# Kernel optimization log

Measured on AMD Instinct MI355X. Metric: run time of the kernel, lower is better.

The kernel has to match this reference:

```python
import jax, jax.numpy as jnp
import numpy as np

NUM_FEATURE = 50


def setup_inputs() -> dict:
    key = jax.random.key(0)
    k1, k2 = jax.random.split(key)
    query = jax.random.normal(k1, (512, NUM_FEATURE), dtype=jnp.float32)
    doc = jax.random.normal(k2, (512, 256, NUM_FEATURE), dtype=jnp.float32)
    # nn.Linear(150, 1, bias=False) with weight filled with 1
    W = jnp.ones((3 * NUM_FEATURE,), dtype=jnp.float32)
    return {"query": query, "doc": doc, "W": W}


def reference(query, doc, W):
    # Split the single 150-dim linear weight into the three trilinear parts:
    # score(x, y) = w1.sen_x + w2.q_y + w3.(sen_x * q_y)
    w1, w2, w3 = W[:NUM_FEATURE], W[NUM_FEATURE:2 * NUM_FEATURE], W[2 * NUM_FEATURE:]
    q_term = query @ w2                      # [Lq]
    qw3 = query * w3                         # [Lq, d]

    def per_sentence(sen):                   # sen: [Ls, d]
        sXY = (sen @ w1)[:, None] + q_term[None, :] + sen @ qw3.T   # [Ls, Lq]
        sD2Q = jax.nn.softmax(sXY, axis=0)   # softmax over sentence tokens
        sQ2D = jax.nn.softmax(sXY, axis=1)   # softmax over query tokens
        aD2Q = sD2Q @ query                  # [Ls, d]
        aQ2D = sD2Q @ (sQ2D.T @ sen)         # (sD2Q @ sQ2D.T) @ sen, cheaper order
        return jnp.concatenate([sen, aD2Q, sen * aD2Q, sen * aQ2D], axis=1)  # [Ls, 4d]

    return jax.vmap(per_sentence)(doc)       # [n_sen, Ls, 4d]
```

## Files before the change

### kernel.cpp

```cpp
#include <hip/hip_runtime.h>
#include <math.h>

typedef __bf16 bf16_t;
typedef bf16_t bf16x2 __attribute__((ext_vector_type(2)));
typedef bf16_t bf16x4 __attribute__((ext_vector_type(4)));
typedef bf16_t bf16x8 __attribute__((ext_vector_type(8)));
typedef float f32x4 __attribute__((ext_vector_type(4)));

#define MFMA16(a,b,c) __builtin_amdgcn_mfma_f32_16x16x32_bf16((a),(b),(c),0,0,0)

#define ND 256
#define NQ 512
#define NF 50
#define L2E 1.44269504f
#define SHIFT 64.0f

#define SENT_E 0
#define PD0_E  16896
#define PD1_E  35328
#define QW3_E  53760
#define QTT_E  62976
#define KL0_E  16896
#define KL1_E  27136
#define EA_B   74752
#define PART_B  144384
#define STATS_B 148480
#define LDS_BYTES 151808

#define ST_QTERM 0
#define ST_CI    512
#define ST_RINV  576

__launch_bounds__(1024, 4)
__global__ void ca10_kernel(const float* __restrict__ query,
                            const float* __restrict__ doc,
                            const float* __restrict__ W,
                            float* __restrict__ out)
{
    extern __shared__ char smem[];
    bf16_t* lb = (bf16_t*)smem;
    float* part  = (float*)(smem + PART_B);
    float* stats = (float*)(smem + STATS_B);

    const int tid = threadIdx.x;
    const int w = tid >> 6, l = tid & 63, ln = l & 15, lg = l >> 4;
    const int s = blockIdx.x;
    const float* sen_g = doc + (size_t)s * (ND * NF);

    auto stageQW3 = [&](int jt, int buf, int tbase, int tn) {
        const int j0 = jt * 64;
        bf16_t* dst = lb + QW3_E + buf * 4608;
        for (int e = tid - tbase; e < 1664; e += tn) {
            int jj = e / 26, c = e - jj * 26;
            if (c < 25) {
                float2 v = ((const float2*)query)[(j0 + jj) * 25 + c];
                bf16x2 p;
                p[0] = (bf16_t)(v.x * W[100 + 2 * c] * L2E);
                p[1] = (bf16_t)(v.y * W[100 + 2 * c + 1] * L2E);
                *(bf16x2*)&dst[jj * 72 + 2 * c] = p;
            } else {
                bf16x2 p;
                p[0] = (bf16_t)(stats[ST_QTERM + j0 + jj] * L2E);
                p[1] = (bf16_t)L2E;
                *(bf16x2*)&dst[jj * 72 + 50] = p;
            }
        }
    };
    auto stageQTT = [&](int jt, int buf, int tbase, int tn) {
        const int j0 = jt * 64;
        bf16_t* dst = lb + QTT_E + buf * 4608;
        for (int e = tid - tbase; e < 1600; e += tn) {
            int c = e >> 6, jj = e & 63;
            float2 v = ((const float2*)query)[(j0 + jj) * 25 + c];
            dst[(2 * c) * 72 + jj]     = (bf16_t)v.x;
            dst[(2 * c + 1) * 72 + jj] = (bf16_t)v.y;
        }
    };

    for (int e = tid; e < 924; e += 1024) {
        int f = 50 + e / 66, c4 = (e - (e / 66) * 66) * 4;
        *(bf16x4*)&lb[SENT_E + f * 264 + c4] = (bf16x4){(bf16_t)0.f,(bf16_t)0.f,(bf16_t)0.f,(bf16_t)0.f};
    }
    for (int e = tid; e < 768; e += 1024) {
        int i = e / 3, c4 = 52 + (e - (e / 3) * 3) * 4;
        *(bf16x4*)&lb[PD0_E + i * 72 + c4] = (bf16x4){(bf16_t)0.f,(bf16_t)0.f,(bf16_t)0.f,(bf16_t)0.f};
    }
    for (int e = tid; e < 384; e += 1024) {
        int b = e / 192, r = e - b * 192;
        int jj = r / 3, c4 = 52 + (r - (r / 3) * 3) * 4;
        *(bf16x4*)&lb[QW3_E + b * 4608 + jj * 72 + c4] = (bf16x4){(bf16_t)0.f,(bf16_t)0.f,(bf16_t)0.f,(bf16_t)0.f};
    }
    for (int e = tid; e < 504; e += 1024) {
        int b = e / 252, r = e - b * 252;
        int f = 50 + r / 18, c4 = (r - (r / 18) * 18) * 4;
        *(bf16x4*)&lb[QTT_E + b * 4608 + f * 72 + c4] = (bf16x4){(bf16_t)0.f,(bf16_t)0.f,(bf16_t)0.f,(bf16_t)0.f};
    }
    for (int e = tid; e < 256 * 25; e += 1024) {
        int i = e / 25, c = e - i * 25;
        float2 v = ((const float2*)sen_g)[i * 25 + c];
        bf16x2 p; p[0] = (bf16_t)v.x; p[1] = (bf16_t)v.y;
        *(bf16x2*)&lb[PD0_E + i * 72 + 2 * c] = p;
        lb[SENT_E + (2 * c) * 264 + i]     = p[0];
        lb[SENT_E + (2 * c + 1) * 264 + i] = p[1];
    }
    if (tid < NQ) {
        float acc = 0.f;
        #pragma unroll
        for (int c = 0; c < 25; ++c) {
            float2 v = ((const float2*)query)[tid * 25 + c];
            acc += v.x * W[NF + 2 * c] + v.y * W[NF + 2 * c + 1];
        }
        stats[ST_QTERM + tid] = acc;
    }
    if (tid < ND) {
        float acc = 0.f;
        #pragma unroll
        for (int f = 0; f < NF; ++f) acc += sen_g[tid * NF + f] * W[f];
        lb[PD0_E + tid * 72 + 50] = (bf16_t)1.0f;
        lb[PD0_E + tid * 72 + 51] = (bf16_t)acc;
    }
    __syncthreads();

    bf16x8 aS[2];
    #pragma unroll
    for (int ks = 0; ks < 2; ++ks)
        aS[ks] = *(bf16x8*)&lb[PD0_E + (w * 16 + ln) * 72 + lg * 8 + ks * 32];
    stageQW3(0, 0, 0, 1024);
    stageQTT(0, 0, 0, 1024);
    __syncthreads();

    f32x4 accD[4];
    f32x4 K[9];
    #pragma unroll
    for (int nf = 0; nf < 4; ++nf) accD[nf] = (f32x4){0.f, 0.f, 0.f, 0.f};
    #pragma unroll
    for (int d = 0; d < 9; ++d) K[d] = (f32x4){0.f, 0.f, 0.f, 0.f};
    float rpart[4] = {0.f, 0.f, 0.f, 0.f};

    auto consumeTile = [&](const bf16_t* pdp, const bf16_t* qtp) {
        bf16x8 aPs[2];
        #pragma unroll
        for (int ks = 0; ks < 2; ++ks) {
            bf16x8 raw = *(bf16x8*)&pdp[(w * 16 + ln) * 72 + lg * 8 + ks * 32];
            float4 c0 = *(const float4*)&stats[ST_CI + lg * 8 + ks * 32];
            float4 c1 = *(const float4*)&stats[ST_CI + lg * 8 + ks * 32 + 4];
            aPs[ks][0] = (bf16_t)((float)raw[0] * c0.x);
            aPs[ks][1] = (bf16_t)((float)raw[1] * c0.y);
            aPs[ks][2] = (bf16_t)((float)raw[2] * c0.z);
            aPs[ks][3] = (bf16_t)((float)raw[3] * c0.w);
            aPs[ks][4] = (bf16_t)((float)raw[4] * c1.x);
            aPs[ks][5] = (bf16_t)((float)raw[5] * c1.y);
            aPs[ks][6] = (bf16_t)((float)raw[6] * c1.z);
            aPs[ks][7] = (bf16_t)((float)raw[7] * c1.w);
        }
        #pragma unroll
        for (int ks = 0; ks < 2; ++ks)
            #pragma unroll
            for (int nf = 0; nf < 4; ++nf) {
                bf16x8 bq = *(bf16x8*)&qtp[(nf * 16 + ln) * 72 + lg * 8 + ks * 32];
                accD[nf] = MFMA16(aPs[ks], bq, accD[nf]);
            }
        #pragma unroll
        for (int d = 0; d < 9; ++d) {
            if (d < 8 || w < 8) {
                const int cb = (w + d) & 15;
                #pragma unroll
                for (int ks = 0; ks < 2; ++ks) {
                    bf16x8 bb = *(bf16x8*)&pdp[(cb * 16 + ln) * 72 + lg * 8 + ks * 32];
                    K[d] = MFMA16(aPs[ks], bb, K[d]);
                }
            }
        }
    };

    for (int jt = 0; jt < 8; ++jt) {
        if (jt > 0) {
            const int pb = (jt - 1) & 1;
            consumeTile(lb + (pb ? PD1_E : PD0_E), lb + QTT_E + pb * 4608);
        }

        const bf16_t* qb = lb + QW3_E + (jt & 1) * 4608;
        bf16_t* pd = lb + ((jt & 1) ? PD1_E : PD0_E);
        #pragma unroll
        for (int hf = 0; hf < 2; ++hf) {
            f32x4 acc[2];
            acc[0] = (f32x4){-SHIFT, -SHIFT, -SHIFT, -SHIFT};
            acc[1] = (f32x4){-SHIFT, -SHIFT, -SHIFT, -SHIFT};
            #pragma unroll
            for (int ks = 0; ks < 2; ++ks)
                #pragma unroll
                for (int h = 0; h < 2; ++h) {
                    const int nf = hf * 2 + h;
                    bf16x8 b = *(bf16x8*)&qb[(nf * 16 + ln) * 72 + lg * 8 + ks * 32];
                    acc[h] = MFMA16(aS[ks], b, acc[h]);
                }
            #pragma unroll
            for (int h = 0; h < 2; ++h) {
                const int nf = hf * 2 + h;
                #pragma unroll
                for (int r = 0; r < 4; ++r) acc[h][r] = exp2f(acc[h][r]);
                float cp = (acc[h][0] + acc[h][1]) + (acc[h][2] + acc[h][3]);
                cp += __shfl_xor(cp, 16);
                cp += __shfl_xor(cp, 32);
                if (lg == 0) part[w * 64 + nf * 16 + ln] = cp;
                #pragma unroll
                for (int r = 0; r < 4; ++r) {
                    rpart[r] += acc[h][r];
                    pd[(w * 16 + lg * 4 + r) * 72 + nf * 16 + ln] = (bf16_t)acc[h][r];
                }
            }
        }
        __syncthreads();

        if (w == 0) {
            float cs = 0.f;
            #pragma unroll
            for (int ww = 0; ww < 16; ++ww) cs += part[ww * 64 + l];
            stats[ST_CI + l] = 1.f / cs;
        } else if (jt < 7) {
            stageQW3(jt + 1, (jt + 1) & 1, 64, 960);
            stageQTT(jt + 1, (jt + 1) & 1, 64, 960);
        }
        __syncthreads();
    }
    consumeTile(lb + PD1_E, lb + QTT_E + 4608);

    #pragma unroll
    for (int r = 0; r < 4; ++r) {
        float v = rpart[r];
        v += __shfl_xor(v, 1);
        v += __shfl_xor(v, 2);
        v += __shfl_xor(v, 4);
        v += __shfl_xor(v, 8);
        if (ln == 0) stats[ST_RINV + w * 16 + lg * 4 + r] = 1.f / v;
    }
    __syncthreads();

    float* ea = (float*)(smem + EA_B);
    #pragma unroll
    for (int nf = 0; nf < 4; ++nf)
        #pragma unroll
        for (int r = 0; r < 4; ++r)
            ea[(w * 16 + lg * 4 + r) * 68 + nf * 16 + ln] = accD[nf][r];

    f32x4 accQ[4];
    #pragma unroll
    for (int nf = 0; nf < 4; ++nf) accQ[nf] = (f32x4){0.f, 0.f, 0.f, 0.f};
    #pragma unroll
    for (int kt = 0; kt < 8; ++kt) {
        bf16_t* kl = lb + ((kt & 1) ? KL1_E : KL0_E);
        #pragma unroll
        for (int d = 0; d < 9; ++d) {
            if (d < 8 || w < 8) {
                const int cb = (w + d) & 15;
                if ((cb >> 1) == kt) {
                    const int h = cb & 1;
                    const float riv = stats[ST_RINV + cb * 16 + ln];
                    #pragma unroll
                    for (int r = 0; r < 4; ++r)
                        kl[(w * 16 + lg * 4 + r) * 40 + h * 16 + ln] =
                            (bf16_t)(K[d][r] * riv);
                }
            }
        }
        if ((w >> 1) == kt) {
            const int h = w & 1;
            float4 rv = *(const float4*)&stats[ST_RINV + w * 16 + lg * 4];
            #pragma unroll
            for (int d = 1; d < 9; ++d) {
                if (d < 8 || w < 8) {
                    const int cb = (w + d) & 15;
                    bf16x4 pk;
                    pk[0] = (bf16_t)(K[d][0] * rv.x);
                    pk[1] = (bf16_t)(K[d][1] * rv.y);
                    pk[2] = (bf16_t)(K[d][2] * rv.z);
                    pk[3] = (bf16_t)(K[d][3] * rv.w);
                    *(bf16x4*)&kl[(cb * 16 + ln) * 40 + h * 16 + lg * 4] = pk;
                }
            }
        }
        __syncthreads();
        bf16x8 aK = *(bf16x8*)&kl[(w * 16 + ln) * 40 + lg * 8];
        #pragma unroll
        for (int nf = 0; nf < 4; ++nf) {
            bf16x8 b = *(bf16x8*)&lb[SENT_E + (nf * 16 + ln) * 264 + kt * 32 + lg * 8];
            accQ[nf] = MFMA16(aK, b, accQ[nf]);
        }
    }
    __syncthreads();

    float* eb = (float*)smem;
    #pragma unroll
    for (int nf = 0; nf < 4; ++nf)
        #pragma unroll
        for (int r = 0; r < 4; ++r)
            eb[(w * 16 + lg * 4 + r) * 68 + nf * 16 + ln] = accQ[nf][r];
    __syncthreads();
    const size_t ob0 = (size_t)s * (ND * 200);
    #pragma unroll
    for (int seg = 0; seg < 4; ++seg) {
        for (int v = tid; v < 6400; v += 1024) {
            int i = v / 25, c = v - (v / 25) * 25;
            int f = 2 * c;
            float2 o;
            if (seg == 0) {
                o = *(const float2*)&sen_g[i * 50 + f];
            } else if (seg == 1) {
                o.x = ea[i * 68 + f]; o.y = ea[i * 68 + f + 1];
            } else if (seg == 2) {
                float2 d = *(const float2*)&sen_g[i * 50 + f];
                o.x = d.x * ea[i * 68 + f]; o.y = d.y * ea[i * 68 + f + 1];
            } else {
                float2 d = *(const float2*)&sen_g[i * 50 + f];
                o.x = d.x * eb[i * 68 + f]; o.y = d.y * eb[i * 68 + f + 1];
            }
            *(float2*)&out[ob0 + (size_t)i * 200 + seg * 50 + f] = o;
        }
    }
}

extern "C" void kernel_launch(void* const* d_in, const int* in_sizes, int n_in,
                              void* d_out, int out_size, void* d_ws, size_t ws_size,
                              hipStream_t stream) {
    const float* query = (const float*)d_in[0];
    const float* doc   = (const float*)d_in[1];
    const float* W     = (const float*)d_in[2];
    float* out = (float*)d_out;
    (void)d_ws; (void)ws_size; (void)n_in; (void)in_sizes; (void)out_size;

    hipFuncSetAttribute((const void*)ca10_kernel,
                        hipFuncAttributeMaxDynamicSharedMemorySize,
                        LDS_BYTES);
    ca10_kernel<<<dim3(512), dim3(1024), LDS_BYTES, stream>>>(query, doc, W, out);
}
```

Measured before the change: 139.1 us.

## Halve block to 8 waves, each computing two 16-row M fragments

Moves from 16 waves handling 16 rows each to 8 waves handling 32 rows each. Every B fragment loaded from LDS now feeds two MFMAs, roughly halving LDS reads per MFMA, and the symmetric K-matrix tiling is regrouped into 32x32 block pairs. The cost is higher register pressure per wave (more accumulators) and fewer waves to hide latency, since LDS use still limits the CU to one block.

```diff
diff --git a/kernel.cpp b/kernel.cpp
--- a/kernel.cpp
+++ b/kernel.cpp
@@ -31,8 +31,8 @@
 #define ST_CI    512
 #define ST_RINV  576
 
-__launch_bounds__(1024, 4)
-__global__ void ca10_kernel(const float* __restrict__ query,
+__launch_bounds__(512, 2)
+__global__ void ca11_kernel(const float* __restrict__ query,
                             const float* __restrict__ doc,
                             const float* __restrict__ W,
                             float* __restrict__ out)
@@ -77,25 +77,25 @@
         }
     };
 
-    for (int e = tid; e < 924; e += 1024) {
+    for (int e = tid; e < 924; e += 512) {
         int f = 50 + e / 66, c4 = (e - (e / 66) * 66) * 4;
         *(bf16x4*)&lb[SENT_E + f * 264 + c4] = (bf16x4){(bf16_t)0.f,(bf16_t)0.f,(bf16_t)0.f,(bf16_t)0.f};
     }
-    for (int e = tid; e < 768; e += 1024) {
+    for (int e = tid; e < 768; e += 512) {
         int i = e / 3, c4 = 52 + (e - (e / 3) * 3) * 4;
         *(bf16x4*)&lb[PD0_E + i * 72 + c4] = (bf16x4){(bf16_t)0.f,(bf16_t)0.f,(bf16_t)0.f,(bf16_t)0.f};
     }
-    for (int e = tid; e < 384; e += 1024) {
+    for (int e = tid; e < 384; e += 512) {
         int b = e / 192, r = e - b * 192;
         int jj = r / 3, c4 = 52 + (r - (r / 3) * 3) * 4;
         *(bf16x4*)&lb[QW3_E + b * 4608 + jj * 72 + c4] = (bf16x4){(bf16_t)0.f,(bf16_t)0.f,(bf16_t)0.f,(bf16_t)0.f};
     }
-    for (int e = tid; e < 504; e += 1024) {
+    for (int e = tid; e < 504; e += 512) {
         int b = e / 252, r = e - b * 252;
         int f = 50 + r / 18, c4 = (r - (r / 18) * 18) * 4;
         *(bf16x4*)&lb[QTT_E + b * 4608 + f * 72 + c4] = (bf16x4){(bf16_t)0.f,(bf16_t)0.f,(bf16_t)0.f,(bf16_t)0.f};
     }
-    for (int e = tid; e < 256 * 25; e += 1024) {
+    for (int e = tid; e < 256 * 25; e += 512) {
         int i = e / 25, c = e - i * 25;
         float2 v = ((const float2*)sen_g)[i * 25 + c];
         bf16x2 p; p[0] = (bf16_t)v.x; p[1] = (bf16_t)v.y;
@@ -103,7 +103,7 @@
         lb[SENT_E + (2 * c) * 264 + i]     = p[0];
         lb[SENT_E + (2 * c + 1) * 264 + i] = p[1];
     }
-    if (tid < NQ) {
+    {
         float acc = 0.f;
         #pragma unroll
         for (int c = 0; c < 25; ++c) {
@@ -121,53 +121,70 @@
     }
     __syncthreads();
 
-    bf16x8 aS[2];
-    #pragma unroll
-    for (int ks = 0; ks < 2; ++ks)
-        aS[ks] = *(bf16x8*)&lb[PD0_E + (w * 16 + ln) * 72 + lg * 8 + ks * 32];
-    stageQW3(0, 0, 0, 1024);
-    stageQTT(0, 0, 0, 1024);
-    __syncthreads();
-
-    f32x4 accD[4];
-    f32x4 K[9];
-    #pragma unroll
-    for (int nf = 0; nf < 4; ++nf) accD[nf] = (f32x4){0.f, 0.f, 0.f, 0.f};
-    #pragma unroll
-    for (int d = 0; d < 9; ++d) K[d] = (f32x4){0.f, 0.f, 0.f, 0.f};
-    float rpart[4] = {0.f, 0.f, 0.f, 0.f};
+    bf16x8 aS[2][2];
+    #pragma unroll
+    for (int mf = 0; mf < 2; ++mf)
+        #pragma unroll
+        for (int ks = 0; ks < 2; ++ks)
+            aS[mf][ks] = *(bf16x8*)&lb[PD0_E + (w * 32 + mf * 16 + ln) * 72 + lg * 8 + ks * 32];
+    stageQW3(0, 0, 0, 512);
+    stageQTT(0, 0, 0, 512);
+    __syncthreads();
+
+    f32x4 accD[2][4];
+    f32x4 K[5][2][2];
+    #pragma unroll
+    for (int mf = 0; mf < 2; ++mf)
+        #pragma unroll
+        for (int nf = 0; nf < 4; ++nf) accD[mf][nf] = (f32x4){0.f, 0.f, 0.f, 0.f};
+    #pragma unroll
+    for (int e = 0; e < 5; ++e)
+        #pragma unroll
+        for (int mf = 0; mf < 2; ++mf)
+            #pragma unroll
+            for (int b = 0; b < 2; ++b) K[e][mf][b] = (f32x4){0.f, 0.f, 0.f, 0.f};
+    float rpart[2][4] = {{0.f,0.f,0.f,0.f},{0.f,0.f,0.f,0.f}};
 
     auto consumeTile = [&](const bf16_t* pdp, const bf16_t* qtp) {
-        bf16x8 aPs[2];
+        bf16x8 aPs[2][2];
         #pragma unroll
         for (int ks = 0; ks < 2; ++ks) {
-            bf16x8 raw = *(bf16x8*)&pdp[(w * 16 + ln) * 72 + lg * 8 + ks * 32];
             float4 c0 = *(const float4*)&stats[ST_CI + lg * 8 + ks * 32];
             float4 c1 = *(const float4*)&stats[ST_CI + lg * 8 + ks * 32 + 4];
-            aPs[ks][0] = (bf16_t)((float)raw[0] * c0.x);
-            aPs[ks][1] = (bf16_t)((float)raw[1] * c0.y);
-            aPs[ks][2] = (bf16_t)((float)raw[2] * c0.z);
-            aPs[ks][3] = (bf16_t)((float)raw[3] * c0.w);
-            aPs[ks][4] = (bf16_t)((float)raw[4] * c1.x);
-            aPs[ks][5] = (bf16_t)((float)raw[5] * c1.y);
-            aPs[ks][6] = (bf16_t)((float)raw[6] * c1.z);
-            aPs[ks][7] = (bf16_t)((float)raw[7] * c1.w);
+            #pragma unroll
+            for (int mf = 0; mf < 2; ++mf) {
+                bf16x8 raw = *(bf16x8*)&pdp[(w * 32 + mf * 16 + ln) * 72 + lg * 8 + ks * 32];
+                aPs[mf][ks][0] = (bf16_t)((float)raw[0] * c0.x);
+                aPs[mf][ks][1] = (bf16_t)((float)raw[1] * c0.y);
+                aPs[mf][ks][2] = (bf16_t)((float)raw[2] * c0.z);
+                aPs[mf][ks][3] = (bf16_t)((float)raw[3] * c0.w);
+                aPs[mf][ks][4] = (bf16_t)((float)raw[4] * c1.x);
+                aPs[mf][ks][5] = (bf16_t)((float)raw[5] * c1.y);
+                aPs[mf][ks][6] = (bf16_t)((float)raw[6] * c1.z);
+                aPs[mf][ks][7] = (bf16_t)((float)raw[7] * c1.w);
+            }
         }
         #pragma unroll
         for (int ks = 0; ks < 2; ++ks)
             #pragma unroll
             for (int nf = 0; nf < 4; ++nf) {
                 bf16x8 bq = *(bf16x8*)&qtp[(nf * 16 + ln) * 72 + lg * 8 + ks * 32];
-                accD[nf] = MFMA16(aPs[ks], bq, accD[nf]);
-            }
-        #pragma unroll
-        for (int d = 0; d < 9; ++d) {
-            if (d < 8 || w < 8) {
-                const int cb = (w + d) & 15;
-                #pragma unroll
-                for (int ks = 0; ks < 2; ++ks) {
-                    bf16x8 bb = *(bf16x8*)&pdp[(cb * 16 + ln) * 72 + lg * 8 + ks * 32];
-                    K[d] = MFMA16(aPs[ks], bb, K[d]);
+                accD[0][nf] = MFMA16(aPs[0][ks], bq, accD[0][nf]);
+                accD[1][nf] = MFMA16(aPs[1][ks], bq, accD[1][nf]);
+            }
+        #pragma unroll
+        for (int e = 0; e < 5; ++e) {
+            if (e < 4 || w < 4) {
+                const int u = (w + e) & 7;
+                #pragma unroll
+                for (int b = 0; b < 2; ++b) {
+                    const int cb = 2 * u + b;
+                    #pragma unroll
+                    for (int ks = 0; ks < 2; ++ks) {
+                        bf16x8 bb = *(bf16x8*)&pdp[(cb * 16 + ln) * 72 + lg * 8 + ks * 32];
+                        K[e][0][b] = MFMA16(aPs[0][ks], bb, K[e][0][b]);
+                        K[e][1][b] = MFMA16(aPs[1][ks], bb, K[e][1][b]);
+                    }
                 }
             }
         }
@@ -183,31 +200,42 @@
         bf16_t* pd = lb + ((jt & 1) ? PD1_E : PD0_E);
         #pragma unroll
         for (int hf = 0; hf < 2; ++hf) {
-            f32x4 acc[2];
-            acc[0] = (f32x4){-SHIFT, -SHIFT, -SHIFT, -SHIFT};
-            acc[1] = (f32x4){-SHIFT, -SHIFT, -SHIFT, -SHIFT};
+            f32x4 sacc[2][2];
+            #pragma unroll
+            for (int mf = 0; mf < 2; ++mf)
+                #pragma unroll
+                for (int h = 0; h < 2; ++h)
+                    sacc[mf][h] = (f32x4){-SHIFT, -SHIFT, -SHIFT, -SHIFT};
             #pragma unroll
             for (int ks = 0; ks < 2; ++ks)
                 #pragma unroll
                 for (int h = 0; h < 2; ++h) {
                     const int nf = hf * 2 + h;
                     bf16x8 b = *(bf16x8*)&qb[(nf * 16 + ln) * 72 + lg * 8 + ks * 32];
-                    acc[h] = MFMA16(aS[ks], b, acc[h]);
+                    sacc[0][h] = MFMA16(aS[0][ks], b, sacc[0][h]);
+                    sacc[1][h] = MFMA16(aS[1][ks], b, sacc[1][h]);
                 }
             #pragma unroll
             for (int h = 0; h < 2; ++h) {
                 const int nf = hf * 2 + h;
                 #pragma unroll
-                for (int r = 0; r < 4; ++r) acc[h][r] = exp2f(acc[h][r]);
-                float cp = (acc[h][0] + acc[h][1]) + (acc[h][2] + acc[h][3]);
+                for (int mf = 0; mf < 2; ++mf)
+                    #pragma unroll
+                    for (int r = 0; r < 4; ++r)
+                        sacc[mf][h][r] = exp2f(sacc[mf][h][r]);
+                float cp = ((sacc[0][h][0] + sacc[0][h][1]) + (sacc[0][h][2] + sacc[0][h][3]))
+                         + ((sacc[1][h][0] + sacc[1][h][1]) + (sacc[1][h][2] + sacc[1][h][3]));
                 cp += __shfl_xor(cp, 16);
                 cp += __shfl_xor(cp, 32);
                 if (lg == 0) part[w * 64 + nf * 16 + ln] = cp;
                 #pragma unroll
-                for (int r = 0; r < 4; ++r) {
-                    rpart[r] += acc[h][r];
-                    pd[(w * 16 + lg * 4 + r) * 72 + nf * 16 + ln] = (bf16_t)acc[h][r];
-                }
+                for (int mf = 0; mf < 2; ++mf)
+                    #pragma unroll
+                    for (int r = 0; r < 4; ++r) {
+                        rpart[mf][r] += sacc[mf][h][r];
+                        pd[(w * 32 + mf * 16 + lg * 4 + r) * 72 + nf * 16 + ln] =
+                            (bf16_t)sacc[mf][h][r];
+                    }
             }
         }
         __syncthreads();
@@ -215,91 +243,108 @@
         if (w == 0) {
             float cs = 0.f;
             #pragma unroll
-            for (int ww = 0; ww < 16; ++ww) cs += part[ww * 64 + l];
+            for (int ww = 0; ww < 8; ++ww) cs += part[ww * 64 + l];
             stats[ST_CI + l] = 1.f / cs;
         } else if (jt < 7) {
-            stageQW3(jt + 1, (jt + 1) & 1, 64, 960);
-            stageQTT(jt + 1, (jt + 1) & 1, 64, 960);
+            stageQW3(jt + 1, (jt + 1) & 1, 64, 448);
+            stageQTT(jt + 1, (jt + 1) & 1, 64, 448);
         }
         __syncthreads();
     }
     consumeTile(lb + PD1_E, lb + QTT_E + 4608);
 
     #pragma unroll
-    for (int r = 0; r < 4; ++r) {
-        float v = rpart[r];
-        v += __shfl_xor(v, 1);
-        v += __shfl_xor(v, 2);
-        v += __shfl_xor(v, 4);
-        v += __shfl_xor(v, 8);
-        if (ln == 0) stats[ST_RINV + w * 16 + lg * 4 + r] = 1.f / v;
-    }
+    for (int mf = 0; mf < 2; ++mf)
+        #pragma unroll
+        for (int r = 0; r < 4; ++r) {
+            float v = rpart[mf][r];
+            v += __shfl_xor(v, 1);
+            v += __shfl_xor(v, 2);
+            v += __shfl_xor(v, 4);
+            v += __shfl_xor(v, 8);
+            if (ln == 0) stats[ST_RINV + w * 32 + mf * 16 + lg * 4 + r] = 1.f / v;
+        }
     __syncthreads();
 
     float* ea = (float*)(smem + EA_B);
     #pragma unroll
-    for (int nf = 0; nf < 4; ++nf)
-        #pragma unroll
-        for (int r = 0; r < 4; ++r)
-            ea[(w * 16 + lg * 4 + r) * 68 + nf * 16 + ln] = accD[nf][r];
-
-    f32x4 accQ[4];
-    #pragma unroll
-    for (int nf = 0; nf < 4; ++nf) accQ[nf] = (f32x4){0.f, 0.f, 0.f, 0.f};
-    #pragma unroll
+    for (int mf = 0; mf < 2; ++mf)
+        #pragma unroll
+        for (int nf = 0; nf < 4; ++nf)
+            #pragma unroll
+            for (int r = 0; r < 4; ++r)
+                ea[(w * 32 + mf * 16 + lg * 4 + r) * 68 + nf * 16 + ln] = accD[mf][nf][r];
+
+    f32x4 accQ[2][4];
+    #pragma unroll
+    for (int mf = 0; mf < 2; ++mf)
+        #pragma unroll
+        for (int nf = 0; nf < 4; ++nf) accQ[mf][nf] = (f32x4){0.f, 0.f, 0.f, 0.f};
+
     for (int kt = 0; kt < 8; ++kt) {
         bf16_t* kl = lb + ((kt & 1) ? KL1_E : KL0_E);
         #pragma unroll
-        for (int d = 0; d < 9; ++d) {
-            if (d < 8 || w < 8) {
-                const int cb = (w + d) & 15;
-                if ((cb >> 1) == kt) {
-                    const int h = cb & 1;
-                    const float riv = stats[ST_RINV + cb * 16 + ln];
+        for (int e = 0; e < 5; ++e) {
+            if ((e < 4 || w < 4) && (((w + e) & 7) == kt)) {
+                #pragma unroll
+                for (int b = 0; b < 2; ++b) {
+                    const float riv = stats[ST_RINV + (2 * kt + b) * 16 + ln];
                     #pragma unroll
-                    for (int r = 0; r < 4; ++r)
-                        kl[(w * 16 + lg * 4 + r) * 40 + h * 16 + ln] =
-                            (bf16_t)(K[d][r] * riv);
+                    for (int mf = 0; mf < 2; ++mf)
+                        #pragma unroll
+                        for (int r = 0; r < 4; ++r)
+                            kl[(w * 32 + mf * 16 + lg * 4 + r) * 40 + b * 16 + ln] =
+                                (bf16_t)(K[e][mf][b][r] * riv);
                 }
             }
         }
-        if ((w >> 1) == kt) {
-            const int h = w & 1;
-            float4 rv = *(const float4*)&stats[ST_RINV + w * 16 + lg * 4];
-            #pragma unroll
-            for (int d = 1; d < 9; ++d) {
-                if (d < 8 || w < 8) {
-                    const int cb = (w + d) & 15;
-                    bf16x4 pk;
-                    pk[0] = (bf16_t)(K[d][0] * rv.x);
-                    pk[1] = (bf16_t)(K[d][1] * rv.y);
-                    pk[2] = (bf16_t)(K[d][2] * rv.z);
-                    pk[3] = (bf16_t)(K[d][3] * rv.w);
-                    *(bf16x4*)&kl[(cb * 16 + ln) * 40 + h * 16 + lg * 4] = pk;
+        if (w == kt) {
+            #pragma unroll
+            for (int mf = 0; mf < 2; ++mf) {
+                float4 rv = *(const float4*)&stats[ST_RINV + w * 32 + mf * 16 + lg * 4];
+                #pragma unroll
+                for (int e = 1; e < 5; ++e) {
+                    if (e < 4 || w < 4) {
+                        const int u = (w + e) & 7;
+                        #pragma unroll
+                        for (int b = 0; b < 2; ++b) {
+                            const int cb = 2 * u + b;
+                            bf16x4 pk;
+                            pk[0] = (bf16_t)(K[e][mf][b][0] * rv.x);
+                            pk[1] = (bf16_t)(K[e][mf][b][1] * rv.y);
+                            pk[2] = (bf16_t)(K[e][mf][b][2] * rv.z);
+                            pk[3] = (bf16_t)(K[e][mf][b][3] * rv.w);
+                            *(bf16x4*)&kl[(cb * 16 + ln) * 40 + mf * 16 + lg * 4] = pk;
+                        }
+                    }
                 }
             }
         }
         __syncthreads();
-        bf16x8 aK = *(bf16x8*)&kl[(w * 16 + ln) * 40 + lg * 8];
+        bf16x8 aK0 = *(bf16x8*)&kl[(w * 32 + ln) * 40 + lg * 8];
+        bf16x8 aK1 = *(bf16x8*)&kl[(w * 32 + 16 + ln) * 40 + lg * 8];
         #pragma unroll
         for (int nf = 0; nf < 4; ++nf) {
             bf16x8 b = *(bf16x8*)&lb[SENT_E + (nf * 16 + ln) * 264 + kt * 32 + lg * 8];
-            accQ[nf] = MFMA16(aK, b, accQ[nf]);
+            accQ[0][nf] = MFMA16(aK0, b, accQ[0][nf]);
+            accQ[1][nf] = MFMA16(aK1, b, accQ[1][nf]);
         }
     }
     __syncthreads();
 
     float* eb = (float*)smem;
     #pragma unroll
-    for (int nf = 0; nf < 4; ++nf)
-        #pragma unroll
-        for (int r = 0; r < 4; ++r)
-            eb[(w * 16 + lg * 4 + r) * 68 + nf * 16 + ln] = accQ[nf][r];
+    for (int mf = 0; mf < 2; ++mf)
+        #pragma unroll
+        for (int nf = 0; nf < 4; ++nf)
+            #pragma unroll
+            for (int r = 0; r < 4; ++r)
+                eb[(w * 32 + mf * 16 + lg * 4 + r) * 68 + nf * 16 + ln] = accQ[mf][nf][r];
     __syncthreads();
     const size_t ob0 = (size_t)s * (ND * 200);
     #pragma unroll
     for (int seg = 0; seg < 4; ++seg) {
-        for (int v = tid; v < 6400; v += 1024) {
+        for (int v = tid; v < 6400; v += 512) {
             int i = v / 25, c = v - (v / 25) * 25;
             int f = 2 * c;
             float2 o;
@@ -328,8 +373,8 @@
     float* out = (float*)d_out;
     (void)d_ws; (void)ws_size; (void)n_in; (void)in_sizes; (void)out_size;
 
-    hipFuncSetAttribute((const void*)ca10_kernel,
+    hipFuncSetAttribute((const void*)ca11_kernel,
                         hipFuncAttributeMaxDynamicSharedMemorySize,
                         LDS_BYTES);
-    ca10_kernel<<<dim3(512), dim3(1024), LDS_BYTES, stream>>>(query, doc, W, out);
+    ca11_kernel<<<dim3(512), dim3(512), LDS_BYTES, stream>>>(query, doc, W, out);
 }
```

Measured after the change: 137.6 us. About the same (-1.1%).
